# Kernel tuning notes

Hardware: AMD Instinct MI355X
Metric: run time of the kernel (lower is better)

The kernel has to match this reference:

```python
import jax, jax.numpy as jnp
import numpy as np

IN_DIM = 8192
OUT_DIM = 8192
BATCH = 2048


def setup_inputs() -> dict:
    key = jax.random.key(0)
    k1, k2, k3, k4 = jax.random.split(key, 4)
    x = jax.random.uniform(k1, (BATCH, IN_DIM), dtype=jnp.float32)  # soft bits in [0,1]
    weights = jax.random.normal(k2, (OUT_DIM, 16), dtype=jnp.float32)
    idx_a = jax.random.randint(k3, (OUT_DIM,), 0, IN_DIM, dtype=jnp.int64)
    idx_b = jax.random.randint(k4, (OUT_DIM,), 0, IN_DIM, dtype=jnp.int64)
    return {"x": x, "weights": weights, "idx_a": idx_a, "idx_b": idx_b}


def _gate_values(a, b):
    # The 16 real-valued relaxations of the 2-input binary logic gates.
    ab = a * b
    return [
        jnp.zeros_like(a),      # 0:  False
        ab,                     # 1:  a AND b
        a - ab,                 # 2:  a AND NOT b
        a,                      # 3:  a
        b - ab,                 # 4:  NOT a AND b
        b,                      # 5:  b
        a + b - 2.0 * ab,       # 6:  a XOR b
        a + b - ab,             # 7:  a OR b
        1.0 - (a + b - ab),     # 8:  NOT (a OR b)
        1.0 - (a + b - 2.0 * ab),  # 9: NOT (a XOR b)
        1.0 - b,                # 10: NOT b
        1.0 - b + ab,           # 11: a OR NOT b
        1.0 - a,                # 12: NOT a
        1.0 - a + ab,           # 13: NOT a OR b
        1.0 - ab,               # 14: NOT (a AND b)
        jnp.ones_like(a),       # 15: True
    ]


def reference(x, weights, idx_a, idx_b):
    # training=True path of LogicLayer.forward_python
    a = x[:, idx_a]  # [B, OUT]
    b = x[:, idx_b]  # [B, OUT]
    w = jax.nn.softmax(weights, axis=-1)  # [OUT, 16]
    gates = _gate_values(a, b)
    out = jnp.zeros_like(a)
    for k in range(16):  # fixed small structural loop over the 16 gates
        out = out + w[None, :, k] * gates[k]
    return out
```

## Files before the change

### kernel.cpp

```cpp
#include <hip/hip_runtime.h>
#include <hip/hip_fp16.h>

#define IN_DIM 8192
#define OUT_DIM 8192
#define BATCH 2048
#define TPB 512
#define NIT (OUT_DIM / 4 / TPB)

typedef float fvec4 __attribute__((ext_vector_type(4)));

#define BAR_LGKM() __asm__ __volatile__("s_waitcnt lgkmcnt(0)\n\ts_barrier" ::: "memory")

__global__ __launch_bounds__(256) void coeff_kernel(
    const float* __restrict__ w,
    const int* __restrict__ idx_a,
    const int* __restrict__ idx_b,
    int* __restrict__ pidx,
    __half2* __restrict__ pc1,
    __half2* __restrict__ pc2)
{
    int j = blockIdx.x * blockDim.x + threadIdx.x;
    if (j >= OUT_DIM) return;

    const float* wj = w + (size_t)j * 16;
    float wv[16];
    float m = -1e30f;
#pragma unroll
    for (int k = 0; k < 16; ++k) { wv[k] = wj[k]; m = fmaxf(m, wv[k]); }
    float s = 0.f;
#pragma unroll
    for (int k = 0; k < 16; ++k) { wv[k] = __expf(wv[k] - m); s += wv[k]; }
    float inv = 1.0f / s;
#pragma unroll
    for (int k = 0; k < 16; ++k) wv[k] *= inv;

    float c0  = wv[8] + wv[9] + wv[10] + wv[11] + wv[12] + wv[13] + wv[14] + wv[15];
    float ca  = wv[2] + wv[3] + wv[6] + wv[7] - wv[8] - wv[9] - wv[12] - wv[13];
    float cb  = wv[4] + wv[5] + wv[6] + wv[7] - wv[8] - wv[9] - wv[10] - wv[11];
    float cab = wv[1] - wv[2] - wv[4] - 2.f * wv[6] - wv[7]
              + wv[8] + 2.f * wv[9] + wv[11] + wv[13] - wv[14];

    pidx[j] = ((idx_a[j] << 2) & 0xffff) | (idx_b[j] << 18);
    pc1[j]  = __floats2half2_rn(c0, ca);
    pc2[j]  = __floats2half2_rn(cb, cab);
}

__global__ __launch_bounds__(TPB, 6) void logic_kernel(
    const float* __restrict__ x,
    const int* __restrict__ pidx,
    const __half2* __restrict__ pc1,
    const __half2* __restrict__ pc2,
    float* __restrict__ out)
{
    __shared__ float xrow[IN_DIM];

    const int row = blockIdx.x;
    const int tid = threadIdx.x;

    const float4* xr4 = (const float4*)(x + (size_t)row * IN_DIM);
    float4 pf0 = xr4[tid];
    float4 pf1 = xr4[TPB + tid];
    float4 pf2 = xr4[2 * TPB + tid];
    float4 pf3 = xr4[3 * TPB + tid];

    const int4* pidx4 = (const int4*)pidx;
    const int4* pc14  = (const int4*)pc1;
    const int4* pc24  = (const int4*)pc2;

    int4 pi = pidx4[tid];
    int4 h1 = pc14[tid];
    int4 h2 = pc24[tid];

    float4* buf4 = (float4*)xrow;
    buf4[tid]           = pf0;
    buf4[TPB + tid]     = pf1;
    buf4[2 * TPB + tid] = pf2;
    buf4[3 * TPB + tid] = pf3;

    BAR_LGKM();

    fvec4* out4 = (fvec4*)(out + (size_t)row * OUT_DIM);

#pragma unroll
    for (int it = 0; it < NIT; ++it) {
        int4 pin = pi, h1n = h1, h2n = h2;
        if (it + 1 < NIT) {
            int j4 = (it + 1) * TPB + tid;
            pin = pidx4[j4];
            h1n = pc14[j4];
            h2n = pc24[j4];
        }

        const char* xb = (const char*)xrow;
        float a0 = *(const float*)(xb + (pi.x & 0xffff)), b0 = *(const float*)(xb + ((unsigned)pi.x >> 16));
        float a1 = *(const float*)(xb + (pi.y & 0xffff)), b1 = *(const float*)(xb + ((unsigned)pi.y >> 16));
        float a2 = *(const float*)(xb + (pi.z & 0xffff)), b2 = *(const float*)(xb + ((unsigned)pi.z >> 16));
        float a3 = *(const float*)(xb + (pi.w & 0xffff)), b3 = *(const float*)(xb + ((unsigned)pi.w >> 16));

        float2 f10 = __half22float2(*(const __half2*)&h1.x);
        float2 f11 = __half22float2(*(const __half2*)&h1.y);
        float2 f12 = __half22float2(*(const __half2*)&h1.z);
        float2 f13 = __half22float2(*(const __half2*)&h1.w);
        float2 f20 = __half22float2(*(const __half2*)&h2.x);
        float2 f21 = __half22float2(*(const __half2*)&h2.y);
        float2 f22 = __half22float2(*(const __half2*)&h2.z);
        float2 f23 = __half22float2(*(const __half2*)&h2.w);

        fvec4 o;
        o.x = f10.x + f10.y * a0 + f20.x * b0 + f20.y * (a0 * b0);
        o.y = f11.x + f11.y * a1 + f21.x * b1 + f21.y * (a1 * b1);
        o.z = f12.x + f12.y * a2 + f22.x * b2 + f22.y * (a2 * b2);
        o.w = f13.x + f13.y * a3 + f23.x * b3 + f23.y * (a3 * b3);
        __builtin_nontemporal_store(o, &out4[it * TPB + tid]);

        pi = pin; h1 = h1n; h2 = h2n;
    }
}

extern "C" void kernel_launch(void* const* d_in, const int* in_sizes, int n_in,
                              void* d_out, int out_size, void* d_ws, size_t ws_size,
                              hipStream_t stream)
{
    const float* x       = (const float*)d_in[0];
    const float* weights = (const float*)d_in[1];
    const int*   idx_a   = (const int*)d_in[2];
    const int*   idx_b   = (const int*)d_in[3];
    float* out = (float*)d_out;

    int*     pidx = (int*)d_ws;
    __half2* pc1  = (__half2*)(pidx + OUT_DIM);
    __half2* pc2  = pc1 + OUT_DIM;

    coeff_kernel<<<OUT_DIM / 256, 256, 0, stream>>>(weights, idx_a, idx_b, pidx, pc1, pc2);
    logic_kernel<<<BATCH, TPB, 0, stream>>>(x, pidx, pc1, pc2, out);
}
```

Baseline: 118.5 us.

## Stage x rows via direct global-to-LDS loads and use fp32 coefficients with FMA

The x row is now copied into shared memory with global_load_lds instructions, which skip the register round trip, and a manual vmcnt wait precedes the barrier. Block size drops from 512 to 256 threads and the occupancy hint changes. The gate coefficients move from packed half2 to float2, which removes the conversions and restructures the output as nested FMAs, but doubles the coefficient traffic. The coeff kernel now reads its weights with vector loads and uses smaller blocks. The hand-set vmcnt(5) depends on how many loads are issued and in what order, which is a correctness risk.

```diff
diff --git a/kernel.cpp b/kernel.cpp
--- a/kernel.cpp
+++ b/kernel.cpp
@@ -4,29 +4,37 @@
 #define IN_DIM 8192
 #define OUT_DIM 8192
 #define BATCH 2048
-#define TPB 512
+#define TPB 256
 #define NIT (OUT_DIM / 4 / TPB)
+#define NSTG (IN_DIM / 4 / TPB)
 
 typedef float fvec4 __attribute__((ext_vector_type(4)));
 
-#define BAR_LGKM() __asm__ __volatile__("s_waitcnt lgkmcnt(0)\n\ts_barrier" ::: "memory")
+#define GLOAD_LDS16(gp, lp)                                                        \
+    __builtin_amdgcn_global_load_lds(                                              \
+        (const __attribute__((address_space(1))) unsigned int*)(gp),               \
+        (__attribute__((address_space(3))) unsigned int*)(lp), 16, 0, 0)
 
-__global__ __launch_bounds__(256) void coeff_kernel(
+__global__ __launch_bounds__(64) void coeff_kernel(
     const float* __restrict__ w,
     const int* __restrict__ idx_a,
     const int* __restrict__ idx_b,
     int* __restrict__ pidx,
-    __half2* __restrict__ pc1,
-    __half2* __restrict__ pc2)
+    float2* __restrict__ pcA,
+    float2* __restrict__ pcB)
 {
-    int j = blockIdx.x * blockDim.x + threadIdx.x;
-    if (j >= OUT_DIM) return;
+    int j = blockIdx.x * 64 + threadIdx.x;
 
-    const float* wj = w + (size_t)j * 16;
-    float wv[16];
+    const float4* w4 = (const float4*)(w + (size_t)j * 16);
+    float4 q0 = w4[0], q1 = w4[1], q2 = w4[2], q3 = w4[3];
+    float wv[16] = { q0.x, q0.y, q0.z, q0.w,
+                     q1.x, q1.y, q1.z, q1.w,
+                     q2.x, q2.y, q2.z, q2.w,
+                     q3.x, q3.y, q3.z, q3.w };
+
     float m = -1e30f;
 #pragma unroll
-    for (int k = 0; k < 16; ++k) { wv[k] = wj[k]; m = fmaxf(m, wv[k]); }
+    for (int k = 0; k < 16; ++k) m = fmaxf(m, wv[k]);
     float s = 0.f;
 #pragma unroll
     for (int k = 0; k < 16; ++k) { wv[k] = __expf(wv[k] - m); s += wv[k]; }
@@ -41,15 +49,15 @@
               + wv[8] + 2.f * wv[9] + wv[11] + wv[13] - wv[14];
 
     pidx[j] = ((idx_a[j] << 2) & 0xffff) | (idx_b[j] << 18);
-    pc1[j]  = __floats2half2_rn(c0, ca);
-    pc2[j]  = __floats2half2_rn(cb, cab);
+    pcA[j]  = make_float2(c0, ca);
+    pcB[j]  = make_float2(cb, cab);
 }
 
-__global__ __launch_bounds__(TPB, 6) void logic_kernel(
+__global__ __launch_bounds__(TPB, 5) void logic_kernel(
     const float* __restrict__ x,
     const int* __restrict__ pidx,
-    const __half2* __restrict__ pc1,
-    const __half2* __restrict__ pc2,
+    const float2* __restrict__ pcA,
+    const float2* __restrict__ pcB,
     float* __restrict__ out)
 {
     __shared__ float xrow[IN_DIM];
@@ -57,63 +65,50 @@
     const int row = blockIdx.x;
     const int tid = threadIdx.x;
 
-    const float4* xr4 = (const float4*)(x + (size_t)row * IN_DIM);
-    float4 pf0 = xr4[tid];
-    float4 pf1 = xr4[TPB + tid];
-    float4 pf2 = xr4[2 * TPB + tid];
-    float4 pf3 = xr4[3 * TPB + tid];
+    const float* xr = x + (size_t)row * IN_DIM;
+#pragma unroll
+    for (int i = 0; i < NSTG; ++i)
+        GLOAD_LDS16(xr + 4 * (i * TPB + tid), xrow + 4 * (i * TPB + tid));
 
-    const int4* pidx4 = (const int4*)pidx;
-    const int4* pc14  = (const int4*)pc1;
-    const int4* pc24  = (const int4*)pc2;
+    asm volatile("" ::: "memory");
 
-    int4 pi = pidx4[tid];
-    int4 h1 = pc14[tid];
-    int4 h2 = pc24[tid];
+    const int4*   pidx4 = (const int4*)pidx;
+    const float4* pA4   = (const float4*)pcA;
+    const float4* pB4   = (const float4*)pcB;
 
-    float4* buf4 = (float4*)xrow;
-    buf4[tid]           = pf0;
-    buf4[TPB + tid]     = pf1;
-    buf4[2 * TPB + tid] = pf2;
-    buf4[3 * TPB + tid] = pf3;
+    int4   pi  = pidx4[tid];
+    float4 cA0 = pA4[2 * tid],     cA1 = pA4[2 * tid + 1];
+    float4 cB0 = pB4[2 * tid],     cB1 = pB4[2 * tid + 1];
 
-    BAR_LGKM();
+    asm volatile("s_waitcnt vmcnt(5)" ::: "memory");
+    __builtin_amdgcn_s_barrier();
 
     fvec4* out4 = (fvec4*)(out + (size_t)row * OUT_DIM);
+    const char* xb = (const char*)xrow;
 
 #pragma unroll
     for (int it = 0; it < NIT; ++it) {
-        int4 pin = pi, h1n = h1, h2n = h2;
+        int4 pin = pi; float4 cA0n = cA0, cA1n = cA1, cB0n = cB0, cB1n = cB1;
         if (it + 1 < NIT) {
             int j4 = (it + 1) * TPB + tid;
-            pin = pidx4[j4];
-            h1n = pc14[j4];
-            h2n = pc24[j4];
+            pin  = pidx4[j4];
+            cA0n = pA4[2 * j4];     cA1n = pA4[2 * j4 + 1];
+            cB0n = pB4[2 * j4];     cB1n = pB4[2 * j4 + 1];
         }
 
-        const char* xb = (const char*)xrow;
         float a0 = *(const float*)(xb + (pi.x & 0xffff)), b0 = *(const float*)(xb + ((unsigned)pi.x >> 16));
         float a1 = *(const float*)(xb + (pi.y & 0xffff)), b1 = *(const float*)(xb + ((unsigned)pi.y >> 16));
         float a2 = *(const float*)(xb + (pi.z & 0xffff)), b2 = *(const float*)(xb + ((unsigned)pi.z >> 16));
         float a3 = *(const float*)(xb + (pi.w & 0xffff)), b3 = *(const float*)(xb + ((unsigned)pi.w >> 16));
 
-        float2 f10 = __half22float2(*(const __half2*)&h1.x);
-        float2 f11 = __half22float2(*(const __half2*)&h1.y);
-        float2 f12 = __half22float2(*(const __half2*)&h1.z);
-        float2 f13 = __half22float2(*(const __half2*)&h1.w);
-        float2 f20 = __half22float2(*(const __half2*)&h2.x);
-        float2 f21 = __half22float2(*(const __half2*)&h2.y);
-        float2 f22 = __half22float2(*(const __half2*)&h2.z);
-        float2 f23 = __half22float2(*(const __half2*)&h2.w);
-
         fvec4 o;
-        o.x = f10.x + f10.y * a0 + f20.x * b0 + f20.y * (a0 * b0);
-        o.y = f11.x + f11.y * a1 + f21.x * b1 + f21.y * (a1 * b1);
-        o.z = f12.x + f12.y * a2 + f22.x * b2 + f22.y * (a2 * b2);
-        o.w = f13.x + f13.y * a3 + f23.x * b3 + f23.y * (a3 * b3);
+        o.x = fmaf(fmaf(cB0.y, a0, cB0.x), b0, fmaf(cA0.y, a0, cA0.x));
+        o.y = fmaf(fmaf(cB0.w, a1, cB0.z), b1, fmaf(cA0.w, a1, cA0.z));
+        o.z = fmaf(fmaf(cB1.y, a2, cB1.x), b2, fmaf(cA1.y, a2, cA1.x));
+        o.w = fmaf(fmaf(cB1.w, a3, cB1.z), b3, fmaf(cA1.w, a3, cA1.z));
         __builtin_nontemporal_store(o, &out4[it * TPB + tid]);
 
-        pi = pin; h1 = h1n; h2 = h2n;
+        pi = pin; cA0 = cA0n; cA1 = cA1n; cB0 = cB0n; cB1 = cB1n;
     }
 }
 
@@ -127,10 +122,10 @@
     const int*   idx_b   = (const int*)d_in[3];
     float* out = (float*)d_out;
 
-    int*     pidx = (int*)d_ws;
-    __half2* pc1  = (__half2*)(pidx + OUT_DIM);
-    __half2* pc2  = pc1 + OUT_DIM;
+    int*    pidx = (int*)d_ws;
+    float2* pcA  = (float2*)(pidx + OUT_DIM);
+    float2* pcB  = pcA + OUT_DIM;
 
-    coeff_kernel<<<OUT_DIM / 256, 256, 0, stream>>>(weights, idx_a, idx_b, pidx, pc1, pc2);
-    logic_kernel<<<BATCH, TPB, 0, stream>>>(x, pidx, pc1, pc2, out);
+    coeff_kernel<<<OUT_DIM / 64, 64, 0, stream>>>(weights, idx_a, idx_b, pidx, pcA, pcB);
+    logic_kernel<<<BATCH, TPB, 0, stream>>>(x, pidx, pcA, pcB, out);
 }
```

Result: slower. 124.5 us (+5.1%).
